# Kernel tuning notes

Measured on AMD Instinct MI355X. Metric: run time of the kernel, lower is better.

Reference implementation:

```python
import jax, jax.numpy as jnp
import numpy as np

N = 50000      # nodes
E = 800000     # edges (avg degree 16)
EL = 200000    # link-prediction pairs
IN = 128       # in_channels
HID = 128      # hidden_conv_2


def setup_inputs() -> dict:
    key = jax.random.key(0)
    ks = jax.random.split(key, 12)
    x = jax.random.normal(ks[0], (N, IN), dtype=jnp.float32)
    edge_index = jax.random.randint(ks[1], (2, E), 0, N, dtype=jnp.int64)
    edge_label_index = jax.random.randint(ks[2], (2, EL), 0, N, dtype=jnp.int64)
    H = jnp.zeros((N, HID), dtype=jnp.float32)
    s_in = 1.0 / np.sqrt(IN)
    s_h = 1.0 / np.sqrt(HID)
    # Stacked ChebConv (K=2) weights for gates [z, r, h]:
    # Wx*: convs on the input x (IN -> HID); Wh*: convs on the state H (HID -> HID)
    Wx0 = jax.random.uniform(ks[3], (3, IN, HID), jnp.float32, -s_in, s_in)
    Wx1 = jax.random.uniform(ks[4], (3, IN, HID), jnp.float32, -s_in, s_in)
    bx = jax.random.uniform(ks[5], (3, HID), jnp.float32, -s_in, s_in)
    Wh0 = jax.random.uniform(ks[6], (3, HID, HID), jnp.float32, -s_h, s_h)
    Wh1 = jax.random.uniform(ks[7], (3, HID, HID), jnp.float32, -s_h, s_h)
    bh = jax.random.uniform(ks[8], (3, HID), jnp.float32, -s_h, s_h)
    post_w = jax.random.uniform(ks[9], (HID, 2), jnp.float32, -s_h, s_h)
    post_b = jax.random.uniform(ks[10], (2,), jnp.float32, -s_h, s_h)
    return {"x": x, "edge_index": edge_index, "edge_label_index": edge_label_index,
            "H": H, "Wx0": Wx0, "Wx1": Wx1, "bx": bx,
            "Wh0": Wh0, "Wh1": Wh1, "bh": bh,
            "post_w": post_w, "post_b": post_b}


def _gconv_gru(x, H, edge_index, Wx0, Wx1, bx, Wh0, Wh1, bh):
    src, dst = edge_index[0], edge_index[1]
    # Symmetric-normalized ChebConv edge weights with lambda_max=2:
    # L_hat = L - I = -D^{-1/2} A D^{-1/2}
    deg = jax.ops.segment_sum(jnp.ones(src.shape[0], x.dtype), src, num_segments=N)
    dinv = jnp.where(deg > 0, jax.lax.rsqrt(jnp.maximum(deg, 1e-12)), 0.0)
    norm = -(dinv[src] * dinv[dst])  # [E]

    def prop(v):  # L_hat @ v via gather-scale-scatter
        return jax.ops.segment_sum(v[src] * norm[:, None], dst, num_segments=N)

    px = prop(x)   # shared Tx_1 for all three x-convs
    pH = prop(H)

    def cheb_x(g):
        return x @ Wx0[g] + px @ Wx1[g] + bx[g]

    def cheb_h(v, pv, g):
        return v @ Wh0[g] + pv @ Wh1[g] + bh[g]

    Z = jax.nn.sigmoid(cheb_x(0) + cheb_h(H, pH, 0))
    R = jax.nn.sigmoid(cheb_x(1) + cheb_h(H, pH, 1))
    HR = H * R
    Ht = jnp.tanh(cheb_x(2) + cheb_h(HR, prop(HR), 2))
    return Z * H + (1.0 - Z) * Ht


def reference(x, edge_index, edge_label_index, H,
              Wx0, Wx1, bx, Wh0, Wh1, bh, post_w, post_b):
    h = _gconv_gru(x, H, edge_index, Wx0, Wx1, bx, Wh0, Wh1, bh)
    hidden = h  # detached copy in the original
    hr = jax.nn.relu(h)
    h_src = hr[edge_label_index[0]]  # [EL, HID]
    h_dst = hr[edge_label_index[1]]
    had = h_src * h_dst
    scores = jnp.sum(had @ post_w + post_b, axis=-1)  # [EL]
    return scores, hidden
```

## Files before the change

### kernel.cpp

```cpp
#include <hip/hip_runtime.h>

#define N_NODES 50000
#define N_EDGES 800000
#define N_EL    200000
#define CH      128

typedef __attribute__((ext_vector_type(8))) short bf16x8;
typedef __attribute__((ext_vector_type(4))) float f32x4;

__device__ __forceinline__ unsigned short f2bf(float f){
  unsigned int u = __float_as_uint(f);
  unsigned int r = (u + 0x7fff + ((u >> 16) & 1)) >> 16;
  return (unsigned short)r;
}
__device__ __forceinline__ float bflo(unsigned int v){ return __uint_as_float(v << 16); }
__device__ __forceinline__ float bfhi(unsigned int v){ return __uint_as_float(v & 0xffff0000u); }
__device__ __forceinline__ float bf2f(unsigned short u){ return __uint_as_float(((unsigned int)u) << 16); }

__device__ __forceinline__ void gload16(const void* g, void* l){
  __builtin_amdgcn_global_load_lds(
      (const __attribute__((address_space(1))) unsigned int*)g,
      (__attribute__((address_space(3))) unsigned int*)l, 16, 0, 0);
}

__global__ void hist_kernel(const int* __restrict__ ei, int* deg, int* cnt){
  int i = blockIdx.x*blockDim.x + threadIdx.x;
  if (i < N_EDGES){
    atomicAdd(&deg[ei[i]], 1);
    atomicAdd(&cnt[ei[N_EDGES + i]], 1);
  }
}

__global__ void dinv_kernel(const int* __restrict__ deg, float* __restrict__ dinv){
  int i = blockIdx.x*blockDim.x + threadIdx.x;
  if (i < N_NODES){
    int d = deg[i];
    dinv[i] = d > 0 ? rsqrtf((float)d) : 0.0f;
  }
}

#define SCAN_NB 196

__global__ void scan_bsum(const int* __restrict__ cnt, int* __restrict__ bsum){
  __shared__ int sh[256];
  int i = blockIdx.x*256 + threadIdx.x;
  sh[threadIdx.x] = (i < N_NODES) ? cnt[i] : 0;
  __syncthreads();
  for (int off = 128; off >= 1; off >>= 1){
    if ((int)threadIdx.x < off) sh[threadIdx.x] += sh[threadIdx.x + off];
    __syncthreads();
  }
  if (threadIdx.x == 0) bsum[blockIdx.x] = sh[0];
}

__global__ void scan_boff(const int* __restrict__ bsum, int* __restrict__ boff){
  __shared__ int sh[256];
  int t = threadIdx.x;
  int v = (t < SCAN_NB) ? bsum[t] : 0;
  sh[t] = v;
  __syncthreads();
  for (int off = 1; off < 256; off <<= 1){
    int tv = (t >= off) ? sh[t - off] : 0;
    __syncthreads();
    sh[t] += tv;
    __syncthreads();
  }
  if (t < SCAN_NB) boff[t] = sh[t] - v;
}

__global__ void scan_final(const int* __restrict__ cnt, const int* __restrict__ boff,
                           int* __restrict__ rowoff, int* __restrict__ cursor){
  __shared__ int sh[256];
  int t = threadIdx.x;
  int i = blockIdx.x*256 + t;
  int v = (i < N_NODES) ? cnt[i] : 0;
  sh[t] = v;
  __syncthreads();
  for (int off = 1; off < 256; off <<= 1){
    int tv = (t >= off) ? sh[t - off] : 0;
    __syncthreads();
    sh[t] += tv;
    __syncthreads();
  }
  int o = boff[blockIdx.x] + sh[t] - v;
  if (i < N_NODES){ rowoff[i] = o; cursor[i] = o; }
  if (i == N_NODES - 1) rowoff[N_NODES] = N_EDGES;
}

__global__ void scatter_kernel(const int* __restrict__ ei, const float* __restrict__ dinv,
                               int* cursor, int* __restrict__ csr_src,
                               float* __restrict__ csr_norm){
  int i = blockIdx.x*blockDim.x + threadIdx.x;
  if (i < N_EDGES){
    int s = ei[i];
    int d = ei[N_EDGES + i];
    int pos = atomicAdd(&cursor[d], 1);
    csr_src[pos]  = s;
    csr_norm[pos] = -(dinv[s] * dinv[d]);
  }
}

__global__ void cvt_xH(const float* __restrict__ x, const float* __restrict__ H,
                       unsigned short* __restrict__ xH){
  const int Q = (N_NODES*CH)/4;
  int i = blockIdx.x*blockDim.x + threadIdx.x;
  if (i >= 2*Q) return;
  const float* src = (i < Q) ? x : H;
  int off = (i < Q) ? i : i - Q;
  float4 v = ((const float4*)src)[off];
  int node = off >> 5, cg = off & 31;
  uint2 o;
  o.x = (unsigned int)f2bf(v.x) | ((unsigned int)f2bf(v.y) << 16);
  o.y = (unsigned int)f2bf(v.z) | ((unsigned int)f2bf(v.w) << 16);
  *(uint2*)(xH + (size_t)node*256 + ((i < Q) ? 0 : 128) + cg*4) = o;
}

__global__ void cvt_w(const float* __restrict__ Wx0, const float* __restrict__ Wx1,
                      const float* __restrict__ Wh0, const float* __restrict__ Wh1,
                      unsigned short* __restrict__ wt){
  int i = blockIdx.x*blockDim.x + threadIdx.x;
  if (i >= 12*128*128) return;
  int m = i >> 14;
  int r = i & 16383;
  int col = r >> 7, k = r & 127;
  const float* W[4] = {Wx0, Wx1, Wh0, Wh1};
  const float* src = W[m/3] + (m%3)*16384;
  wt[i] = f2bf(src[k*128 + col]);
}

__global__ void prop_x2(const int* __restrict__ rowoff, const int* __restrict__ csr_src,
                        const float* __restrict__ csr_norm,
                        const unsigned short* __restrict__ xH,
                        unsigned short* __restrict__ px, unsigned short* __restrict__ pH){
  int node = blockIdx.x*4 + ((int)threadIdx.x >> 6);
  if (node >= N_NODES) return;
  int lane = threadIdx.x & 63;
  int half = lane >> 5, il = lane & 31;
  const unsigned short* base = xH + half*128 + il*4;
  int beg = rowoff[node], end = rowoff[node+1];
  float a0 = 0.f, a1 = 0.f, a2 = 0.f, a3 = 0.f;
  int k = beg;
  for (; k + 4 <= end; k += 4){
    int s0 = csr_src[k], s1 = csr_src[k+1], s2 = csr_src[k+2], s3 = csr_src[k+3];
    float w0 = csr_norm[k], w1 = csr_norm[k+1], w2 = csr_norm[k+2], w3 = csr_norm[k+3];
    uint2 v0 = *(const uint2*)(base + (size_t)s0*256);
    uint2 v1 = *(const uint2*)(base + (size_t)s1*256);
    uint2 v2 = *(const uint2*)(base + (size_t)s2*256);
    uint2 v3 = *(const uint2*)(base + (size_t)s3*256);
    a0 += w0*bflo(v0.x) + w1*bflo(v1.x) + w2*bflo(v2.x) + w3*bflo(v3.x);
    a1 += w0*bfhi(v0.x) + w1*bfhi(v1.x) + w2*bfhi(v2.x) + w3*bfhi(v3.x);
    a2 += w0*bflo(v0.y) + w1*bflo(v1.y) + w2*bflo(v2.y) + w3*bflo(v3.y);
    a3 += w0*bfhi(v0.y) + w1*bfhi(v1.y) + w2*bfhi(v2.y) + w3*bfhi(v3.y);
  }
  for (; k < end; ++k){
    int s = csr_src[k];
    float w = csr_norm[k];
    uint2 v = *(const uint2*)(base + (size_t)s*256);
    a0 += w*bflo(v.x); a1 += w*bfhi(v.x);
    a2 += w*bflo(v.y); a3 += w*bfhi(v.y);
  }
  uint2 o;
  o.x = (unsigned int)f2bf(a0) | ((unsigned int)f2bf(a1) << 16);
  o.y = (unsigned int)f2bf(a2) | ((unsigned int)f2bf(a3) << 16);
  unsigned short* O = (half ? pH : px) + (size_t)node*CH + il*4;
  *(uint2*)O = o;
}

__global__ void prop_one(const int* __restrict__ rowoff, const int* __restrict__ csr_src,
                         const float* __restrict__ csr_norm,
                         const unsigned short* __restrict__ V,
                         unsigned short* __restrict__ O){
  int node = blockIdx.x*4 + ((int)threadIdx.x >> 6);
  if (node >= N_NODES) return;
  int lane = threadIdx.x & 63;
  const unsigned short* base = V + lane*2;
  int beg = rowoff[node], end = rowoff[node+1];
  float a0 = 0.f, a1 = 0.f;
  int k = beg;
  for (; k + 4 <= end; k += 4){
    int s0 = csr_src[k], s1 = csr_src[k+1], s2 = csr_src[k+2], s3 = csr_src[k+3];
    float w0 = csr_norm[k], w1 = csr_norm[k+1], w2 = csr_norm[k+2], w3 = csr_norm[k+3];
    unsigned int v0 = *(const unsigned int*)(base + (size_t)s0*256);
    unsigned int v1 = *(const unsigned int*)(base + (size_t)s1*256);
    unsigned int v2 = *(const unsigned int*)(base + (size_t)s2*256);
    unsigned int v3 = *(const unsigned int*)(base + (size_t)s3*256);
    a0 += w0*bflo(v0) + w1*bflo(v1) + w2*bflo(v2) + w3*bflo(v3);
    a1 += w0*bfhi(v0) + w1*bfhi(v1) + w2*bfhi(v2) + w3*bfhi(v3);
  }
  for (; k < end; ++k){
    int s = csr_src[k];
    float w = csr_norm[k];
    unsigned int v = *(const unsigned int*)(base + (size_t)s*256);
    a0 += w*bflo(v); a1 += w*bfhi(v);
  }
  *(unsigned int*)(O + (size_t)node*CH + lane*2) =
      (unsigned int)f2bf(a0) | ((unsigned int)f2bf(a1) << 16);
}

__launch_bounds__(256, 3)
__global__ void mfma_gates(unsigned short* xH,
                           const unsigned short* __restrict__ px,
                           const unsigned short* __restrict__ pH,
                           const unsigned short* __restrict__ wt,
                           const float* __restrict__ bx, const float* __restrict__ bh,
                           unsigned short* __restrict__ zb,
                           float* __restrict__ pre2){
  __shared__ unsigned short lds[2][3][4096];
  const int M = 128*128;
  int lane = threadIdx.x & 63;
  int w    = threadIdx.x >> 6;
  int lr   = lane & 15;
  int kq   = lane >> 4;
  int r0w  = blockIdx.x*64 + w*16;
  int rA   = min(r0w + lr, N_NODES - 1);

  const unsigned short* Am[4] = {xH, px, xH + 128, pH};
  const int strA[4] = {256, 128, 256, 128};

  const int scol = lane >> 2;
  const int skbe = (((lane & 3) ^ ((lane >> 3) & 3)) << 3);
  auto stage = [&](int s, int b){
    int t = s >> 2, ko = (s & 3) * 32;
    int nm = (t < 2) ? 3 : 2;
    for (int q = w; q < nm*8; q += 4){
      int g = q >> 3, i = q & 7;
      const unsigned short* src = wt + (size_t)(t*3 + g)*M
                                + (size_t)(i*16 + scol)*CH + ko + skbe;
      gload16(src, &lds[b][g][i*512]);
    }
  };

  f32x4 accZ[8], accR[8], accP[8];
  #pragma unroll
  for (int c = 0; c < 8; ++c){
    accZ[c] = (f32x4){0.f,0.f,0.f,0.f};
    accR[c] = (f32x4){0.f,0.f,0.f,0.f};
    accP[c] = (f32x4){0.f,0.f,0.f,0.f};
  }

  const int rdo = ((kq ^ ((lr >> 1) & 3)) << 3);

  stage(0, 0);
  __syncthreads();
  #pragma unroll
  for (int s = 0; s < 16; ++s){
    const int b = s & 1;
    if (s < 15) stage(s + 1, b ^ 1);
    const int t = s >> 2, ko = (s & 3) * 32;
    bf16x8 a = *(const bf16x8*)(Am[t] + (size_t)rA*strA[t] + ko + kq*8);
    #pragma unroll
    for (int c = 0; c < 8; ++c){
      bf16x8 bz = *(const bf16x8*)&lds[b][0][(c*16 + lr)*32 + rdo];
      bf16x8 br = *(const bf16x8*)&lds[b][1][(c*16 + lr)*32 + rdo];
      accZ[c] = __builtin_amdgcn_mfma_f32_16x16x32_bf16(a, bz, accZ[c], 0, 0, 0);
      accR[c] = __builtin_amdgcn_mfma_f32_16x16x32_bf16(a, br, accR[c], 0, 0, 0);
      if (t < 2){
        bf16x8 bp = *(const bf16x8*)&lds[b][2][(c*16 + lr)*32 + rdo];
        accP[c] = __builtin_amdgcn_mfma_f32_16x16x32_bf16(a, bp, accP[c], 0, 0, 0);
      }
    }
    __syncthreads();
  }

  float bsZ[8], bsR[8], bsP[8];
  #pragma unroll
  for (int c = 0; c < 8; ++c){
    int col = c*16 + lr;
    bsZ[c] = bx[col]       + bh[col];
    bsR[c] = bx[128 + col] + bh[128 + col];
    bsP[c] = bx[256 + col];
  }

  #pragma unroll
  for (int j = 0; j < 4; ++j){
    int row = r0w + kq*4 + j;
    if (row >= N_NODES) continue;
    size_t ro = (size_t)row * CH;
    size_t rh = (size_t)row * 256 + 128;
    #pragma unroll
    for (int c = 0; c < 8; ++c){
      int col = c*16 + lr;
      float z = 1.0f/(1.0f + __expf(-(accZ[c][j] + bsZ[c])));
      float r = 1.0f/(1.0f + __expf(-(accR[c][j] + bsR[c])));
      float h = bf2f(xH[rh + col]);
      zb[ro + col]   = f2bf(z);
      xH[rh + col]   = f2bf(h * r);
      pre2[ro + col] = accP[c][j] + bsP[c];
    }
  }
}

__launch_bounds__(256, 3)
__global__ void mfma_final(const unsigned short* __restrict__ hr,
                           const unsigned short* __restrict__ phr,
                           const unsigned short* __restrict__ B0,
                           const unsigned short* __restrict__ B1,
                           const float* __restrict__ bias,
                           const float* __restrict__ Hp, const float* __restrict__ pre2,
                           const unsigned short* __restrict__ zb,
                           float* __restrict__ hidden,
                           unsigned short* __restrict__ relu_b){
  __shared__ unsigned short lds[2][4096];
  int lane = threadIdx.x & 63;
  int w    = threadIdx.x >> 6;
  int lr   = lane & 15;
  int kq   = lane >> 4;
  int r0w  = blockIdx.x*64 + w*16;
  int rA   = min(r0w + lr, N_NODES - 1);

  const unsigned short* Am[2] = {hr, phr};
  const int strA[2] = {256, 128};

  const int scol = lane >> 2;
  const int skbe = (((lane & 3) ^ ((lane >> 3) & 3)) << 3);
  auto stage = [&](int s, int b){
    int t = s >> 2, ko = (s & 3) * 32;
    const unsigned short* B = t ? B1 : B0;
    for (int q = w; q < 8; q += 4){
      const unsigned short* src = B + (size_t)(q*16 + scol)*CH + ko + skbe;
      gload16(src, &lds[b][q*512]);
    }
  };

  f32x4 acc[8];
  #pragma unroll
  for (int c = 0; c < 8; ++c) acc[c] = (f32x4){0.f,0.f,0.f,0.f};

  const int rdo = ((kq ^ ((lr >> 1) & 3)) << 3);

  stage(0, 0);
  __syncthreads();
  #pragma unroll
  for (int s = 0; s < 8; ++s){
    const int b = s & 1;
    if (s < 7) stage(s + 1, b ^ 1);
    const int t = s >> 2, ko = (s & 3) * 32;
    bf16x8 a = *(const bf16x8*)(Am[t] + (size_t)rA*strA[t] + ko + kq*8);
    #pragma unroll
    for (int c = 0; c < 8; ++c){
      bf16x8 bb = *(const bf16x8*)&lds[b][(c*16 + lr)*32 + rdo];
      acc[c] = __builtin_amdgcn_mfma_f32_16x16x32_bf16(a, bb, acc[c], 0, 0, 0);
    }
    __syncthreads();
  }

  float bs[8];
  #pragma unroll
  for (int c = 0; c < 8; ++c) bs[c] = bias[c*16 + lr];

  #pragma unroll
  for (int j = 0; j < 4; ++j){
    int row = r0w + kq*4 + j;
    if (row >= N_NODES) continue;
    size_t ro = (size_t)row * CH;
    #pragma unroll
    for (int c = 0; c < 8; ++c){
      size_t o = ro + c*16 + lr;
      float ht = tanhf(acc[c][j] + bs[c] + pre2[o]);
      float z  = bf2f(zb[o]);
      float h  = z*Hp[o] + (1.0f - z)*ht;
      hidden[o] = h;
      relu_b[o] = f2bf(fmaxf(h, 0.0f));
    }
  }
}

__global__ void scores_bf16(const int* __restrict__ eli, const unsigned short* __restrict__ hr,
                            const float* __restrict__ pw, const float* __restrict__ pb,
                            float* __restrict__ out){
  __shared__ float sw[CH];
  int t = threadIdx.x;
  if (t < CH) sw[t] = pw[2*t] + pw[2*t + 1];
  __syncthreads();
  int pair = blockIdx.x*16 + (t >> 4);
  if (pair >= N_EL) return;
  int il = t & 15;
  int a = eli[pair];
  int b = eli[N_EL + pair];
  bf16x8 va = *(const bf16x8*)(hr + (size_t)a*CH + il*8);
  bf16x8 vb = *(const bf16x8*)(hr + (size_t)b*CH + il*8);
  float s = 0.f;
  #pragma unroll
  for (int j = 0; j < 8; ++j){
    s += bf2f((unsigned short)va[j]) * bf2f((unsigned short)vb[j]) * sw[il*8 + j];
  }
  s += __shfl_xor(s, 1, 64);
  s += __shfl_xor(s, 2, 64);
  s += __shfl_xor(s, 4, 64);
  s += __shfl_xor(s, 8, 64);
  if (il == 0) out[pair] = s + pb[0] + pb[1];
}

extern "C" void kernel_launch(void* const* d_in, const int* in_sizes, int n_in,
                              void* d_out, int out_size, void* d_ws, size_t ws_size,
                              hipStream_t stream) {
  const float* x   = (const float*)d_in[0];
  const int*   ei  = (const int*)d_in[1];
  const int*   eli = (const int*)d_in[2];
  const float* H   = (const float*)d_in[3];
  const float* Wx0 = (const float*)d_in[4];
  const float* Wx1 = (const float*)d_in[5];
  const float* bx  = (const float*)d_in[6];
  const float* Wh0 = (const float*)d_in[7];
  const float* Wh1 = (const float*)d_in[8];
  const float* bh  = (const float*)d_in[9];
  const float* pw  = (const float*)d_in[10];
  const float* pb  = (const float*)d_in[11];
  float* out    = (float*)d_out;
  float* scores = out;
  float* hidden = out + N_EL;

  char* w = (char*)d_ws;
  auto alloc = [&](size_t b){ void* p = (void*)w; w += (b + 255) & ~(size_t)255; return p; };
  int*   deg      = (int*)  alloc((size_t)N_NODES*4);
  int*   cnt      = (int*)  alloc((size_t)N_NODES*4);
  float* dinv     = (float*)alloc((size_t)N_NODES*4);
  int*   rowoff   = (int*)  alloc((size_t)(N_NODES+1)*4);
  int*   cursor   = (int*)  alloc((size_t)N_NODES*4);
  int*   bsum     = (int*)  alloc((size_t)SCAN_NB*4);
  int*   boff     = (int*)  alloc((size_t)SCAN_NB*4);
  int*   csr_src  = (int*)  alloc((size_t)N_EDGES*4);
  float* csr_norm = (float*)alloc((size_t)N_EDGES*4);
  unsigned short* wt  = (unsigned short*)alloc((size_t)12*128*128*2);
  unsigned short* xHb = (unsigned short*)alloc((size_t)N_NODES*256*2);
  unsigned short* pxb = (unsigned short*)alloc((size_t)N_NODES*CH*2);
  unsigned short* pHb = (unsigned short*)alloc((size_t)N_NODES*CH*2);
  unsigned short* zbb = (unsigned short*)alloc((size_t)N_NODES*CH*2);
  float* pre2 = (float*)alloc((size_t)N_NODES*CH*4);
  unsigned short* pHRb   = pHb;
  unsigned short* relu_b = pxb;

  hipMemsetAsync(deg, 0, (size_t)N_NODES*4, stream);
  hipMemsetAsync(cnt, 0, (size_t)N_NODES*4, stream);

  hist_kernel<<<(N_EDGES+255)/256, 256, 0, stream>>>(ei, deg, cnt);
  dinv_kernel<<<(N_NODES+255)/256, 256, 0, stream>>>(deg, dinv);
  scan_bsum <<<SCAN_NB, 256, 0, stream>>>(cnt, bsum);
  scan_boff <<<1, 256, 0, stream>>>(bsum, boff);
  scan_final<<<SCAN_NB, 256, 0, stream>>>(cnt, boff, rowoff, cursor);
  scatter_kernel<<<(N_EDGES+255)/256, 256, 0, stream>>>(ei, dinv, cursor, csr_src, csr_norm);

  cvt_xH<<<(((N_NODES*CH)/4)*2 + 255)/256, 256, 0, stream>>>(x, H, xHb);
  cvt_w <<<(12*128*128 + 255)/256, 256, 0, stream>>>(Wx0, Wx1, Wh0, Wh1, wt);

  prop_x2<<<(N_NODES+3)/4, 256, 0, stream>>>(rowoff, csr_src, csr_norm, xHb, pxb, pHb);

  const int GB = (N_NODES + 63) / 64;
  const size_t M = 128*128;
  mfma_gates<<<GB, 256, 0, stream>>>(xHb, pxb, pHb, wt, bx, bh, zbb, pre2);
  prop_one<<<(N_NODES+3)/4, 256, 0, stream>>>(rowoff, csr_src, csr_norm, xHb + 128, pHRb);
  mfma_final<<<GB, 256, 0, stream>>>(xHb + 128, pHRb, wt + 8*M, wt + 11*M,
      bh + 256, H, pre2, zbb, hidden, relu_b);

  scores_bf16<<<(N_EL+15)/16, 256, 0, stream>>>(eli, relu_b, pw, pb, scores);
}
```

Baseline: 444.7 us.

## Keep weight fragments in registers and loop persistent blocks over row tiles

```diff
diff --git a/kernel.cpp b/kernel.cpp
--- a/kernel.cpp
+++ b/kernel.cpp
@@ -4,6 +4,7 @@
 #define N_EDGES 800000
 #define N_EL    200000
 #define CH      128
+#define NTILES  3125
 
 typedef __attribute__((ext_vector_type(8))) short bf16x8;
 typedef __attribute__((ext_vector_type(4))) float f32x4;
@@ -16,12 +17,6 @@
 __device__ __forceinline__ float bflo(unsigned int v){ return __uint_as_float(v << 16); }
 __device__ __forceinline__ float bfhi(unsigned int v){ return __uint_as_float(v & 0xffff0000u); }
 __device__ __forceinline__ float bf2f(unsigned short u){ return __uint_as_float(((unsigned int)u) << 16); }
-
-__device__ __forceinline__ void gload16(const void* g, void* l){
-  __builtin_amdgcn_global_load_lds(
-      (const __attribute__((address_space(1))) unsigned int*)g,
-      (__attribute__((address_space(3))) unsigned int*)l, 16, 0, 0);
-}
 
 __global__ void hist_kernel(const int* __restrict__ ei, int* deg, int* cnt){
   int i = blockIdx.x*blockDim.x + threadIdx.x;
@@ -197,166 +192,120 @@
       (unsigned int)f2bf(a0) | ((unsigned int)f2bf(a1) << 16);
 }
 
-__launch_bounds__(256, 3)
-__global__ void mfma_gates(unsigned short* xH,
-                           const unsigned short* __restrict__ px,
-                           const unsigned short* __restrict__ pH,
-                           const unsigned short* __restrict__ wt,
-                           const float* __restrict__ bx, const float* __restrict__ bh,
-                           unsigned short* __restrict__ zb,
-                           float* __restrict__ pre2){
-  __shared__ unsigned short lds[2][3][4096];
+__launch_bounds__(512, 2)
+__global__ void mfma_gates2(unsigned short* xH,
+                            const unsigned short* __restrict__ px,
+                            const unsigned short* __restrict__ pH,
+                            const unsigned short* __restrict__ wt,
+                            const float* __restrict__ bx, const float* __restrict__ bh,
+                            unsigned short* __restrict__ zb,
+                            float* __restrict__ pre2){
   const int M = 128*128;
   int lane = threadIdx.x & 63;
   int w    = threadIdx.x >> 6;
   int lr   = lane & 15;
   int kq   = lane >> 4;
-  int r0w  = blockIdx.x*64 + w*16;
-  int rA   = min(r0w + lr, N_NODES - 1);
+  int mycol = w*16 + lr;
 
   const unsigned short* Am[4] = {xH, px, xH + 128, pH};
   const int strA[4] = {256, 128, 256, 128};
 
-  const int scol = lane >> 2;
-  const int skbe = (((lane & 3) ^ ((lane >> 3) & 3)) << 3);
-  auto stage = [&](int s, int b){
-    int t = s >> 2, ko = (s & 3) * 32;
-    int nm = (t < 2) ? 3 : 2;
-    for (int q = w; q < nm*8; q += 4){
-      int g = q >> 3, i = q & 7;
-      const unsigned short* src = wt + (size_t)(t*3 + g)*M
-                                + (size_t)(i*16 + scol)*CH + ko + skbe;
-      gload16(src, &lds[b][g][i*512]);
-    }
-  };
-
-  f32x4 accZ[8], accR[8], accP[8];
+  bf16x8 BZ[16], BR[16], BP[8];
   #pragma unroll
-  for (int c = 0; c < 8; ++c){
-    accZ[c] = (f32x4){0.f,0.f,0.f,0.f};
-    accR[c] = (f32x4){0.f,0.f,0.f,0.f};
-    accP[c] = (f32x4){0.f,0.f,0.f,0.f};
-  }
-
-  const int rdo = ((kq ^ ((lr >> 1) & 3)) << 3);
-
-  stage(0, 0);
-  __syncthreads();
-  #pragma unroll
-  for (int s = 0; s < 16; ++s){
-    const int b = s & 1;
-    if (s < 15) stage(s + 1, b ^ 1);
-    const int t = s >> 2, ko = (s & 3) * 32;
-    bf16x8 a = *(const bf16x8*)(Am[t] + (size_t)rA*strA[t] + ko + kq*8);
-    #pragma unroll
-    for (int c = 0; c < 8; ++c){
-      bf16x8 bz = *(const bf16x8*)&lds[b][0][(c*16 + lr)*32 + rdo];
-      bf16x8 br = *(const bf16x8*)&lds[b][1][(c*16 + lr)*32 + rdo];
-      accZ[c] = __builtin_amdgcn_mfma_f32_16x16x32_bf16(a, bz, accZ[c], 0, 0, 0);
-      accR[c] = __builtin_amdgcn_mfma_f32_16x16x32_bf16(a, br, accR[c], 0, 0, 0);
-      if (t < 2){
-        bf16x8 bp = *(const bf16x8*)&lds[b][2][(c*16 + lr)*32 + rdo];
-        accP[c] = __builtin_amdgcn_mfma_f32_16x16x32_bf16(a, bp, accP[c], 0, 0, 0);
+  for (int t = 0; t < 4; ++t){
+    #pragma unroll
+    for (int q = 0; q < 4; ++q){
+      const unsigned short* base = wt + (size_t)(t*3)*M + (size_t)mycol*CH + q*32 + kq*8;
+      BZ[t*4+q] = *(const bf16x8*)(base);
+      BR[t*4+q] = *(const bf16x8*)(base + M);
+      if (t < 2) BP[t*4+q] = *(const bf16x8*)(base + 2*M);
+    }
+  }
+
+  float bsZ = bx[mycol]       + bh[mycol];
+  float bsR = bx[128 + mycol] + bh[128 + mycol];
+  float bsP = bx[256 + mycol];
+
+  for (int tile = blockIdx.x; tile < NTILES; tile += gridDim.x){
+    int r0 = tile * 16;
+    int rA = r0 + lr;
+    f32x4 accZ = (f32x4){0.f,0.f,0.f,0.f};
+    f32x4 accR = (f32x4){0.f,0.f,0.f,0.f};
+    f32x4 accP = (f32x4){0.f,0.f,0.f,0.f};
+    #pragma unroll
+    for (int t = 0; t < 4; ++t){
+      const unsigned short* Ap = Am[t] + (size_t)rA*strA[t] + kq*8;
+      #pragma unroll
+      for (int q = 0; q < 4; ++q){
+        bf16x8 a = *(const bf16x8*)(Ap + q*32);
+        accZ = __builtin_amdgcn_mfma_f32_16x16x32_bf16(a, BZ[t*4+q], accZ, 0, 0, 0);
+        accR = __builtin_amdgcn_mfma_f32_16x16x32_bf16(a, BR[t*4+q], accR, 0, 0, 0);
+        if (t < 2)
+          accP = __builtin_amdgcn_mfma_f32_16x16x32_bf16(a, BP[t*4+q], accP, 0, 0, 0);
       }
     }
-    __syncthreads();
-  }
-
-  float bsZ[8], bsR[8], bsP[8];
-  #pragma unroll
-  for (int c = 0; c < 8; ++c){
-    int col = c*16 + lr;
-    bsZ[c] = bx[col]       + bh[col];
-    bsR[c] = bx[128 + col] + bh[128 + col];
-    bsP[c] = bx[256 + col];
-  }
-
-  #pragma unroll
-  for (int j = 0; j < 4; ++j){
-    int row = r0w + kq*4 + j;
-    if (row >= N_NODES) continue;
-    size_t ro = (size_t)row * CH;
-    size_t rh = (size_t)row * 256 + 128;
-    #pragma unroll
-    for (int c = 0; c < 8; ++c){
-      int col = c*16 + lr;
-      float z = 1.0f/(1.0f + __expf(-(accZ[c][j] + bsZ[c])));
-      float r = 1.0f/(1.0f + __expf(-(accR[c][j] + bsR[c])));
-      float h = bf2f(xH[rh + col]);
-      zb[ro + col]   = f2bf(z);
-      xH[rh + col]   = f2bf(h * r);
-      pre2[ro + col] = accP[c][j] + bsP[c];
-    }
-  }
-}
-
-__launch_bounds__(256, 3)
-__global__ void mfma_final(const unsigned short* __restrict__ hr,
-                           const unsigned short* __restrict__ phr,
-                           const unsigned short* __restrict__ B0,
-                           const unsigned short* __restrict__ B1,
-                           const float* __restrict__ bias,
-                           const float* __restrict__ Hp, const float* __restrict__ pre2,
-                           const unsigned short* __restrict__ zb,
-                           float* __restrict__ hidden,
-                           unsigned short* __restrict__ relu_b){
-  __shared__ unsigned short lds[2][4096];
+    #pragma unroll
+    for (int j = 0; j < 4; ++j){
+      int row = r0 + kq*4 + j;
+      size_t ro = (size_t)row*CH + mycol;
+      size_t rh = (size_t)row*256 + 128 + mycol;
+      float z = 1.0f/(1.0f + __expf(-(accZ[j] + bsZ)));
+      float r = 1.0f/(1.0f + __expf(-(accR[j] + bsR)));
+      float h = bf2f(xH[rh]);
+      zb[ro]   = f2bf(z);
+      xH[rh]   = f2bf(h * r);
+      pre2[ro] = accP[j] + bsP;
+    }
+  }
+}
+
+__launch_bounds__(512, 2)
+__global__ void mfma_final2(const unsigned short* __restrict__ hr,
+                            const unsigned short* __restrict__ phr,
+                            const unsigned short* __restrict__ B0,
+                            const unsigned short* __restrict__ B1,
+                            const float* __restrict__ bias,
+                            const float* __restrict__ Hp, const float* __restrict__ pre2,
+                            const unsigned short* __restrict__ zb,
+                            float* __restrict__ hidden,
+                            unsigned short* __restrict__ relu_b){
   int lane = threadIdx.x & 63;
   int w    = threadIdx.x >> 6;
   int lr   = lane & 15;
   int kq   = lane >> 4;
-  int r0w  = blockIdx.x*64 + w*16;
-  int rA   = min(r0w + lr, N_NODES - 1);
+  int mycol = w*16 + lr;
 
   const unsigned short* Am[2] = {hr, phr};
   const int strA[2] = {256, 128};
 
-  const int scol = lane >> 2;
-  const int skbe = (((lane & 3) ^ ((lane >> 3) & 3)) << 3);
-  auto stage = [&](int s, int b){
-    int t = s >> 2, ko = (s & 3) * 32;
-    const unsigned short* B = t ? B1 : B0;
-    for (int q = w; q < 8; q += 4){
-      const unsigned short* src = B + (size_t)(q*16 + scol)*CH + ko + skbe;
-      gload16(src, &lds[b][q*512]);
-    }
-  };
-
-  f32x4 acc[8];
+  bf16x8 BF[8];
   #pragma unroll
-  for (int c = 0; c < 8; ++c) acc[c] = (f32x4){0.f,0.f,0.f,0.f};
-
-  const int rdo = ((kq ^ ((lr >> 1) & 3)) << 3);
-
-  stage(0, 0);
-  __syncthreads();
-  #pragma unroll
-  for (int s = 0; s < 8; ++s){
-    const int b = s & 1;
-    if (s < 7) stage(s + 1, b ^ 1);
-    const int t = s >> 2, ko = (s & 3) * 32;
-    bf16x8 a = *(const bf16x8*)(Am[t] + (size_t)rA*strA[t] + ko + kq*8);
-    #pragma unroll
-    for (int c = 0; c < 8; ++c){
-      bf16x8 bb = *(const bf16x8*)&lds[b][(c*16 + lr)*32 + rdo];
-      acc[c] = __builtin_amdgcn_mfma_f32_16x16x32_bf16(a, bb, acc[c], 0, 0, 0);
-    }
-    __syncthreads();
-  }
-
-  float bs[8];
-  #pragma unroll
-  for (int c = 0; c < 8; ++c) bs[c] = bias[c*16 + lr];
-
-  #pragma unroll
-  for (int j = 0; j < 4; ++j){
-    int row = r0w + kq*4 + j;
-    if (row >= N_NODES) continue;
-    size_t ro = (size_t)row * CH;
-    #pragma unroll
-    for (int c = 0; c < 8; ++c){
-      size_t o = ro + c*16 + lr;
-      float ht = tanhf(acc[c][j] + bs[c] + pre2[o]);
+  for (int t = 0; t < 2; ++t){
+    #pragma unroll
+    for (int q = 0; q < 4; ++q){
+      const unsigned short* B = t ? B1 : B0;
+      BF[t*4+q] = *(const bf16x8*)(B + (size_t)mycol*CH + q*32 + kq*8);
+    }
+  }
+  float bs = bias[mycol];
+
+  for (int tile = blockIdx.x; tile < NTILES; tile += gridDim.x){
+    int r0 = tile * 16;
+    int rA = r0 + lr;
+    f32x4 acc0 = (f32x4){0.f,0.f,0.f,0.f};
+    f32x4 acc1 = (f32x4){0.f,0.f,0.f,0.f};
+    #pragma unroll
+    for (int q = 0; q < 4; ++q){
+      bf16x8 a0 = *(const bf16x8*)(Am[0] + (size_t)rA*256 + q*32 + kq*8);
+      bf16x8 a1 = *(const bf16x8*)(Am[1] + (size_t)rA*128 + q*32 + kq*8);
+      acc0 = __builtin_amdgcn_mfma_f32_16x16x32_bf16(a0, BF[q],   acc0, 0, 0, 0);
+      acc1 = __builtin_amdgcn_mfma_f32_16x16x32_bf16(a1, BF[4+q], acc1, 0, 0, 0);
+    }
+    #pragma unroll
+    for (int j = 0; j < 4; ++j){
+      int row = r0 + kq*4 + j;
+      size_t o = (size_t)row*CH + mycol;
+      float ht = tanhf(acc0[j] + acc1[j] + bs + pre2[o]);
       float z  = bf2f(zb[o]);
       float h  = z*Hp[o] + (1.0f - z)*ht;
       hidden[o] = h;
@@ -445,11 +394,10 @@
 
   prop_x2<<<(N_NODES+3)/4, 256, 0, stream>>>(rowoff, csr_src, csr_norm, xHb, pxb, pHb);
 
-  const int GB = (N_NODES + 63) / 64;
   const size_t M = 128*128;
-  mfma_gates<<<GB, 256, 0, stream>>>(xHb, pxb, pHb, wt, bx, bh, zbb, pre2);
+  mfma_gates2<<<512, 512, 0, stream>>>(xHb, pxb, pHb, wt, bx, bh, zbb, pre2);
   prop_one<<<(N_NODES+3)/4, 256, 0, stream>>>(rowoff, csr_src, csr_norm, xHb + 128, pHRb);
-  mfma_final<<<GB, 256, 0, stream>>>(xHb + 128, pHRb, wt + 8*M, wt + 11*M,
+  mfma_final2<<<512, 512, 0, stream>>>(xHb + 128, pHRb, wt + 8*M, wt + 11*M,
       bh + 256, H, pre2, zbb, hidden, relu_b);
 
   scores_bf16<<<(N_EL+15)/16, 256, 0, stream>>>(eli, relu_b, pw, pb, scores);
```

Measured after the change: 467.0 us. 1.05x slower.
